# Kernel tuning notes

Measured on AMD Instinct MI355X. Metric: run time of the kernel, lower is better.

The kernel has to match this reference:

```python
import jax, jax.numpy as jnp
import numpy as np

B, T, I, H, O = 64, 1024, 256, 512, 128


def setup_inputs() -> dict:
    key = jax.random.key(0)
    ks = jax.random.split(key, 12)
    s = 1.0 / np.sqrt(H)  # PyTorch LSTM init: U(-1/sqrt(H), 1/sqrt(H))
    u = lambda k, shape: jax.random.uniform(k, shape, jnp.float32, -s, s)
    return {
        "inputs": jax.random.normal(ks[0], (B, T, I), jnp.float32),
        "W_ih_f": u(ks[1], (4 * H, I)),
        "W_hh_f": u(ks[2], (4 * H, H)),
        "b_ih_f": u(ks[3], (4 * H,)),
        "b_hh_f": u(ks[4], (4 * H,)),
        "W_ih_b": u(ks[5], (4 * H, I)),
        "W_hh_b": u(ks[6], (4 * H, H)),
        "b_ih_b": u(ks[7], (4 * H,)),
        "b_hh_b": u(ks[8], (4 * H,)),
        "W_out": u(ks[9], (O, 2 * H)),
        "b_out": u(ks[10], (O,)),
    }


def _lstm_dir(inputs, W_ih, W_hh, b_ih, b_hh, reverse):
    # Precompute input contribution for all timesteps: [B,T,4H] -> [T,B,4H]
    xg = jnp.einsum("bti,gi->btg", inputs, W_ih) + b_ih + b_hh
    xg = jnp.swapaxes(xg, 0, 1)
    b = inputs.shape[0]
    h0 = jnp.zeros((b, H), inputs.dtype)
    c0 = jnp.zeros((b, H), inputs.dtype)

    def step(carry, x_t):
        h, c = carry
        gates = x_t + h @ W_hh.T  # [B,4H], PyTorch gate order i,f,g,o
        i, f, g, o = jnp.split(gates, 4, axis=-1)
        i = jax.nn.sigmoid(i)
        f = jax.nn.sigmoid(f)
        g = jnp.tanh(g)
        o = jax.nn.sigmoid(o)
        c = f * c + i * g
        h = o * jnp.tanh(c)
        return (h, c), h

    (hT, cT), hs = jax.lax.scan(step, (h0, c0), xg, reverse=reverse)
    return jnp.swapaxes(hs, 0, 1), hT, cT  # hs: [B,T,H]


def reference(inputs, W_ih_f, W_hh_f, b_ih_f, b_hh_f,
              W_ih_b, W_hh_b, b_ih_b, b_hh_b, W_out, b_out):
    y_f, h_f, c_f = _lstm_dir(inputs, W_ih_f, W_hh_f, b_ih_f, b_hh_f, False)
    y_b, h_b, c_b = _lstm_dir(inputs, W_ih_b, W_hh_b, b_ih_b, b_hh_b, True)
    y = jnp.concatenate([y_f, y_b], axis=-1)            # [B,T,2H]
    out = jnp.einsum("bth,oh->bto", y, W_out) + b_out    # [B,T,O]
    h_n = jnp.stack([h_f, h_b])                          # [2,B,H]
    c_n = jnp.stack([c_f, c_b])                          # [2,B,H]
    return out, h_n, c_n
```

## Files before the change

### kernel.cpp

```cpp
#include <hip/hip_runtime.h>
#include <stdint.h>

#define T_LEN 1024
#define B_SZ  64
#define I_SZ  256
#define H_SZ  512
#define O_SZ  128

#define HB_OFF  0ull
#define Y_OFF   1048576ull
#define XBF_OFF 135266304ull
#define MEMSET_BYTES 1048576ull

typedef __attribute__((ext_vector_type(8))) short short8;
typedef __attribute__((ext_vector_type(4))) float f32x4;

__device__ __forceinline__ unsigned short f2bf(float f) {
  unsigned u = __float_as_uint(f);
  u += 0x7fffu + ((u >> 16) & 1u);
  return (unsigned short)(u >> 16);
}
__device__ __forceinline__ ushort4 cvt4(float4 v) {
  ushort4 p;
  p.x = f2bf(v.x); p.y = f2bf(v.y); p.z = f2bf(v.z); p.w = f2bf(v.w);
  return p;
}
__device__ __forceinline__ float sigm(float x) { return 1.0f / (1.0f + __expf(-x)); }
__device__ __forceinline__ float tanh_f(float x) { return 1.0f - 2.0f / (1.0f + __expf(2.0f * x)); }

__global__ void __launch_bounds__(256) cvt_x(const float* __restrict__ x,
                                             unsigned short* __restrict__ xb) {
  size_t i = ((size_t)blockIdx.x * 256 + threadIdx.x) * 8;
  float4 a = *(const float4*)(x + i);
  float4 b = *(const float4*)(x + i + 4);
  *(ushort4*)(xb + i)     = cvt4(a);
  *(ushort4*)(xb + i + 4) = cvt4(b);
}

__global__ void __launch_bounds__(512, 2)
lstm_scan(const unsigned short* __restrict__ xbf,
          const float* __restrict__ WihF, const float* __restrict__ WhhF,
          const float* __restrict__ bihF, const float* __restrict__ bhhF,
          const float* __restrict__ WihB, const float* __restrict__ WhhB,
          const float* __restrict__ bihB, const float* __restrict__ bhhB,
          unsigned char* __restrict__ ws, float* __restrict__ out)
{
  __shared__ unsigned short xs[2][16][264];
  __shared__ unsigned short hs[16][520];
  __shared__ float gbuf[4][16][36];
  __shared__ float cst[16][36];

  const int tid  = threadIdx.x;
  const int lane = tid & 63;
  const int wave = tid >> 6;
  const int nl   = lane & 15;
  const int q16  = lane >> 4;

  const int wg = blockIdx.x;
  const int d  = wg >> 6;
  const int b0 = ((wg >> 4) & 3) * 16;
  const int u0 = (wg & 15) * 32;

  const float* Wih = d ? WihB : WihF;
  const float* Whh = d ? WhhB : WhhF;
  const float* bih = d ? bihB : bihF;
  const float* bhh = d ? bhhB : bhhF;

  const int gate = wave >> 1;
  const int usub = (wave & 1) * 16;

  short8 wfrag[24];
  {
    const int row = gate * H_SZ + u0 + usub + nl;
    const float* wi = Wih + (size_t)row * I_SZ;
    const float* wh = Whh + (size_t)row * H_SZ;
#pragma unroll
    for (int kk = 0; kk < 24; ++kk) {
      const float* src = (kk < 8) ? (wi + kk * 32 + q16 * 8)
                                  : (wh + (kk - 8) * 32 + q16 * 8);
      float4 v0 = ((const float4*)src)[0];
      float4 v1 = ((const float4*)src)[1];
      short8 w;
      w[0] = (short)f2bf(v0.x); w[1] = (short)f2bf(v0.y);
      w[2] = (short)f2bf(v0.z); w[3] = (short)f2bf(v0.w);
      w[4] = (short)f2bf(v1.x); w[5] = (short)f2bf(v1.y);
      w[6] = (short)f2bf(v1.z); w[7] = (short)f2bf(v1.w);
      wfrag[kk] = w;
    }
  }
  const float bias = bih[gate * H_SZ + u0 + usub + nl] + bhh[gate * H_SZ + u0 + usub + nl];

  cst[tid >> 5][tid & 31] = 0.0f;

  unsigned* hbuf32 = (unsigned*)(ws + HB_OFF);
  unsigned* ybuf32 = (unsigned*)(ws + Y_OFF);
  unsigned* hs32   = (unsigned*)hs;

  const int sm = tid >> 5, sseg = tid & 31;

  {
    const int t0 = d ? (T_LEN - 1) : 0;
    uint4 a = *(const uint4*)(xbf + ((size_t)(b0 + sm) * T_LEN + t0) * I_SZ + sseg * 8);
    *(uint4*)(&xs[0][sm][sseg * 8]) = a;
  }
  __syncthreads();
  f32x4 xacc = {0.f, 0.f, 0.f, 0.f};
  {
    const unsigned short* xr = &xs[0][nl][q16 * 8];
#pragma unroll
    for (int kk = 0; kk < 8; ++kk) {
      short8 a = *(const short8*)(xr + kk * 32);
      xacc = __builtin_amdgcn_mfma_f32_16x16x32_bf16(a, wfrag[kk], xacc, 0, 0, 0);
    }
  }
  uint4 px;
  {
    const int t1 = d ? (T_LEN - 2) : 1;
    px = *(const uint4*)(xbf + ((size_t)(b0 + sm) * T_LEN + t1) * I_SZ + sseg * 8);
  }

  for (int s = 0; s < T_LEN; ++s) {
    const int t   = d ? (T_LEN - 1 - s) : s;
    const int cur = s & 1, nxt = cur ^ 1;
    const int rb  = cur ^ 1, wb = cur;

    unsigned wlo[8], whi[8];
    const unsigned* hb = hbuf32 + (size_t)((rb * 2 + d) * B_SZ + b0) * 512;
#pragma unroll
    for (int j = 0; j < 8; ++j) {
      int lin2 = j * 512 + tid;
      int m = lin2 >> 8, p = lin2 & 255;
      wlo[j] = __hip_atomic_load(hb + m * 512 + 2 * p,     __ATOMIC_RELAXED, __HIP_MEMORY_SCOPE_AGENT);
      whi[j] = __hip_atomic_load(hb + m * 512 + 2 * p + 1, __ATOMIC_RELAXED, __HIP_MEMORY_SCOPE_AGENT);
    }
    if (s < T_LEN - 1)
      *(uint4*)(&xs[nxt][sm][sseg * 8]) = px;
    {
      const unsigned tag = (unsigned)s;
      for (;;) {
        unsigned bad = 0;
#pragma unroll
        for (int j = 0; j < 8; ++j)
          bad |= (((wlo[j] ^ tag) | (whi[j] ^ tag)) & 0xffffu) ? (1u << j) : 0u;
        if (!bad) break;
#pragma unroll
        for (int j = 0; j < 8; ++j)
          if (bad & (1u << j)) {
            int lin2 = j * 512 + tid;
            int m = lin2 >> 8, p = lin2 & 255;
            wlo[j] = __hip_atomic_load(hb + m * 512 + 2 * p,     __ATOMIC_RELAXED, __HIP_MEMORY_SCOPE_AGENT);
            whi[j] = __hip_atomic_load(hb + m * 512 + 2 * p + 1, __ATOMIC_RELAXED, __HIP_MEMORY_SCOPE_AGENT);
          }
      }
    }
#pragma unroll
    for (int j = 0; j < 8; ++j) {
      int lin2 = j * 512 + tid;
      int m = lin2 >> 8, p = lin2 & 255;
      hs32[m * 260 + p] = (wlo[j] >> 16) | (whi[j] & 0xffff0000u);
    }
    __syncthreads();

    f32x4 acc0 = xacc, acc1 = {0.f, 0.f, 0.f, 0.f};
    {
      const unsigned short* ar = &hs[nl][q16 * 8];
#pragma unroll
      for (int kk = 0; kk < 16; kk += 2) {
        short8 a0 = *(const short8*)(ar + kk * 32);
        short8 a1 = *(const short8*)(ar + (kk + 1) * 32);
        acc0 = __builtin_amdgcn_mfma_f32_16x16x32_bf16(a0, wfrag[8 + kk], acc0, 0, 0, 0);
        acc1 = __builtin_amdgcn_mfma_f32_16x16x32_bf16(a1, wfrag[9 + kk], acc1, 0, 0, 0);
      }
      acc0 += acc1;
    }

#pragma unroll
    for (int r = 0; r < 4; ++r) {
      float v = acc0[r] + bias;
      v = (gate == 2) ? tanh_f(v) : sigm(v);
      gbuf[gate][q16 * 4 + r][usub + nl] = v;
    }
    __syncthreads();

    {
      int m = tid >> 5, n = tid & 31;
      float gi = gbuf[0][m][n], gf = gbuf[1][m][n];
      float gg = gbuf[2][m][n], go = gbuf[3][m][n];
      float c = gf * cst[m][n] + gi * gg;
      cst[m][n] = c;
      float h = go * tanh_f(c);
      unsigned hbits = f2bf(h);
      __hip_atomic_store(hbuf32 + (size_t)((wb * 2 + d) * B_SZ + b0 + m) * 512 + u0 + n,
                         (hbits << 16) | (unsigned)(s + 1),
                         __ATOMIC_RELAXED, __HIP_MEMORY_SCOPE_AGENT);
      unsigned other = __shfl_xor(hbits, 1);
      if ((tid & 1) == 0) {
        unsigned packed = hbits | (other << 16);
        size_t yi = ((size_t)(b0 + m) * T_LEN + t) * 512 + (d * H_SZ + u0 + n) / 2;
        ybuf32[yi] = packed;
      }
      if (s == T_LEN - 1) {
        size_t hi = (size_t)(d * B_SZ + b0 + m) * H_SZ + u0 + n;
        out[8388608ull + hi] = h;
        out[8388608ull + 65536ull + hi] = c;
      }
    }

    if (s < T_LEN - 1) {
      if (s + 2 < T_LEN) {
        const int t2 = d ? (T_LEN - 3 - s) : (s + 2);
        px = *(const uint4*)(xbf + ((size_t)(b0 + sm) * T_LEN + t2) * I_SZ + sseg * 8);
      }
      f32x4 xa = {0.f, 0.f, 0.f, 0.f};
      const unsigned short* xr = &xs[nxt][nl][q16 * 8];
#pragma unroll
      for (int kk = 0; kk < 8; ++kk) {
        short8 a = *(const short8*)(xr + kk * 32);
        xa = __builtin_amdgcn_mfma_f32_16x16x32_bf16(a, wfrag[kk], xa, 0, 0, 0);
      }
      xacc = xa;
    }
  }
}

__global__ void __launch_bounds__(256, 1)
proj(const unsigned short* __restrict__ y, const float* __restrict__ Wout,
     const float* __restrict__ bout, float* __restrict__ out)
{
  __shared__ unsigned short ys[128 * 264];
  __shared__ unsigned short wst[128 * 264];

  const int tid  = threadIdx.x;
  const int wave = tid >> 6;
  const int lane = tid & 63;
  const int nl   = lane & 15;
  const int q16  = lane >> 4;
  const int m0   = blockIdx.x * 128;

  f32x4 acc[2][8];
#pragma unroll
  for (int a = 0; a < 2; ++a)
#pragma unroll
    for (int b = 0; b < 8; ++b) acc[a][b] = (f32x4){0.f, 0.f, 0.f, 0.f};

  for (int k0 = 0; k0 < 1024; k0 += 256) {
    {
      int r = tid >> 1, half = tid & 1;
      const uint4* src = (const uint4*)(y + (size_t)(m0 + r) * 1024 + k0 + half * 128);
      uint4* dst = (uint4*)(ys + r * 264 + half * 128);
#pragma unroll
      for (int q = 0; q < 16; ++q) dst[q] = src[q];
    }
    {
      int r = tid >> 1, half = tid & 1;
      const float4* src = (const float4*)(Wout + (size_t)r * 1024 + k0 + half * 128);
      unsigned short* wd = wst + r * 264 + half * 128;
#pragma unroll
      for (int q = 0; q < 32; ++q) *(ushort4*)(wd + q * 4) = cvt4(src[q]);
    }
    __syncthreads();

#pragma unroll
    for (int kk = 0; kk < 8; ++kk) {
      const int ko = kk * 32 + q16 * 8;
      short8 bfr[8];
#pragma unroll
      for (int nt = 0; nt < 8; ++nt)
        bfr[nt] = *(const short8*)(wst + (nt * 16 + nl) * 264 + ko);
#pragma unroll
      for (int mtt = 0; mtt < 2; ++mtt) {
        short8 a = *(const short8*)(ys + ((wave * 2 + mtt) * 16 + nl) * 264 + ko);
#pragma unroll
        for (int nt = 0; nt < 8; ++nt)
          acc[mtt][nt] = __builtin_amdgcn_mfma_f32_16x16x32_bf16(a, bfr[nt], acc[mtt][nt], 0, 0, 0);
      }
    }
    __syncthreads();
  }

#pragma unroll
  for (int mtt = 0; mtt < 2; ++mtt) {
#pragma unroll
    for (int nt = 0; nt < 8; ++nt) {
      int col = nt * 16 + nl;
      float bo = bout[col];
      int rowb = m0 + (wave * 2 + mtt) * 16 + q16 * 4;
#pragma unroll
      for (int r = 0; r < 4; ++r)
        out[(size_t)(rowb + r) * O_SZ + col] = acc[mtt][nt][r] + bo;
    }
  }
}

extern "C" void kernel_launch(void* const* d_in, const int* in_sizes, int n_in,
                              void* d_out, int out_size, void* d_ws, size_t ws_size,
                              hipStream_t stream) {
  const float* x    = (const float*)d_in[0];
  const float* WihF = (const float*)d_in[1];
  const float* WhhF = (const float*)d_in[2];
  const float* bihF = (const float*)d_in[3];
  const float* bhhF = (const float*)d_in[4];
  const float* WihB = (const float*)d_in[5];
  const float* WhhB = (const float*)d_in[6];
  const float* bihB = (const float*)d_in[7];
  const float* bhhB = (const float*)d_in[8];
  const float* Wout = (const float*)d_in[9];
  const float* bout = (const float*)d_in[10];
  float* out = (float*)d_out;
  unsigned char* ws = (unsigned char*)d_ws;

  hipMemsetAsync(ws, 0, (size_t)MEMSET_BYTES, stream);
  cvt_x<<<8192, 256, 0, stream>>>(x, (unsigned short*)(ws + XBF_OFF));
  lstm_scan<<<128, 512, 0, stream>>>((const unsigned short*)(ws + XBF_OFF),
                                     WihF, WhhF, bihF, bhhF,
                                     WihB, WhhB, bihB, bhhB,
                                     ws, out);
  proj<<<512, 256, 0, stream>>>((const unsigned short*)(ws + Y_OFF), Wout, bout, out);
}
```

Baseline: 3.267 ms.

## Interleave two batch halves per workgroup and shuffle gates in registers

Each workgroup now handles two 16-row batch halves in alternation, and the grid shrinks from 128 to 64 blocks. While one half waits on the cross-block h flags, the other half's recurrent GEMM and pointwise math can run, hiding the inter-block sync latency. Weight rows are reordered so the four gates of a unit fall in adjacent lanes and are combined with xor shuffles. This removes the gbuf shared-memory round trip, one barrier per step, and the x staging in LDS. The cost is half as many CUs doing twice the serial work per step, and a polling loop that now includes s_sleep.

```diff
diff --git a/kernel.cpp b/kernel.cpp
--- a/kernel.cpp
+++ b/kernel.cpp
@@ -45,33 +45,31 @@
           const float* __restrict__ bihB, const float* __restrict__ bhhB,
           unsigned char* __restrict__ ws, float* __restrict__ out)
 {
-  __shared__ unsigned short xs[2][16][264];
-  __shared__ unsigned short hs[16][520];
-  __shared__ float gbuf[4][16][36];
-  __shared__ float cst[16][36];
+  __shared__ unsigned short hs[2][16][520];
 
   const int tid  = threadIdx.x;
   const int lane = tid & 63;
   const int wave = tid >> 6;
   const int nl   = lane & 15;
   const int q16  = lane >> 4;
-
-  const int wg = blockIdx.x;
-  const int d  = wg >> 6;
-  const int b0 = ((wg >> 4) & 3) * 16;
-  const int u0 = (wg & 15) * 32;
+  const int uu   = nl >> 2;
+  const int gt   = nl & 3;
+  const int mrow = q16 * 4 + gt;
+
+  const int wg   = blockIdx.x;
+  const int d    = wg >> 5;
+  const int pair = (wg >> 4) & 1;
+  const int u0   = (wg & 15) * 32;
+  const int u    = u0 + wave * 4 + uu;
+  const int row  = gt * H_SZ + u;
 
   const float* Wih = d ? WihB : WihF;
   const float* Whh = d ? WhhB : WhhF;
   const float* bih = d ? bihB : bihF;
   const float* bhh = d ? bhhB : bhhF;
 
-  const int gate = wave >> 1;
-  const int usub = (wave & 1) * 16;
-
   short8 wfrag[24];
   {
-    const int row = gate * H_SZ + u0 + usub + nl;
     const float* wi = Wih + (size_t)row * I_SZ;
     const float* wh = Whh + (size_t)row * H_SZ;
 #pragma unroll
@@ -88,137 +86,147 @@
       wfrag[kk] = w;
     }
   }
-  const float bias = bih[gate * H_SZ + u0 + usub + nl] + bhh[gate * H_SZ + u0 + usub + nl];
-
-  cst[tid >> 5][tid & 31] = 0.0f;
+  const float bias = bih[row] + bhh[row];
 
   unsigned* hbuf32 = (unsigned*)(ws + HB_OFF);
   unsigned* ybuf32 = (unsigned*)(ws + Y_OFF);
-  unsigned* hs32   = (unsigned*)hs;
-
-  const int sm = tid >> 5, sseg = tid & 31;
-
-  {
+
+  const int b0h2[2] = { pair * 32, pair * 32 + 16 };
+  float cstr[2] = {0.f, 0.f};
+  f32x4 xacc[2];
+
+#pragma unroll
+  for (int half = 0; half < 2; ++half) {
     const int t0 = d ? (T_LEN - 1) : 0;
-    uint4 a = *(const uint4*)(xbf + ((size_t)(b0 + sm) * T_LEN + t0) * I_SZ + sseg * 8);
-    *(uint4*)(&xs[0][sm][sseg * 8]) = a;
-  }
-  __syncthreads();
-  f32x4 xacc = {0.f, 0.f, 0.f, 0.f};
-  {
-    const unsigned short* xr = &xs[0][nl][q16 * 8];
+    const unsigned short* xr =
+        xbf + ((size_t)(b0h2[half] + nl) * T_LEN + t0) * I_SZ + q16 * 8;
+    f32x4 xa = {0.f, 0.f, 0.f, 0.f};
 #pragma unroll
     for (int kk = 0; kk < 8; ++kk) {
       short8 a = *(const short8*)(xr + kk * 32);
-      xacc = __builtin_amdgcn_mfma_f32_16x16x32_bf16(a, wfrag[kk], xacc, 0, 0, 0);
-    }
-  }
-  uint4 px;
-  {
-    const int t1 = d ? (T_LEN - 2) : 1;
-    px = *(const uint4*)(xbf + ((size_t)(b0 + sm) * T_LEN + t1) * I_SZ + sseg * 8);
+      xa = __builtin_amdgcn_mfma_f32_16x16x32_bf16(a, wfrag[kk], xa, 0, 0, 0);
+    }
+    xacc[half] = xa;
+  }
+
+  unsigned wlo[8], whi[8];
+  const unsigned* hb = hbuf32 + (size_t)((1 * 2 + d) * B_SZ + b0h2[0]) * 512;
+#pragma unroll
+  for (int j = 0; j < 8; ++j) {
+    int lin2 = j * 512 + tid, mm = lin2 >> 8, pp = lin2 & 255;
+    wlo[j] = __hip_atomic_load(hb + mm * 512 + 2 * pp,     __ATOMIC_RELAXED, __HIP_MEMORY_SCOPE_AGENT);
+    whi[j] = __hip_atomic_load(hb + mm * 512 + 2 * pp + 1, __ATOMIC_RELAXED, __HIP_MEMORY_SCOPE_AGENT);
   }
 
   for (int s = 0; s < T_LEN; ++s) {
-    const int t   = d ? (T_LEN - 1 - s) : s;
-    const int cur = s & 1, nxt = cur ^ 1;
-    const int rb  = cur ^ 1, wb = cur;
-
-    unsigned wlo[8], whi[8];
-    const unsigned* hb = hbuf32 + (size_t)((rb * 2 + d) * B_SZ + b0) * 512;
-#pragma unroll
-    for (int j = 0; j < 8; ++j) {
-      int lin2 = j * 512 + tid;
-      int m = lin2 >> 8, p = lin2 & 255;
-      wlo[j] = __hip_atomic_load(hb + m * 512 + 2 * p,     __ATOMIC_RELAXED, __HIP_MEMORY_SCOPE_AGENT);
-      whi[j] = __hip_atomic_load(hb + m * 512 + 2 * p + 1, __ATOMIC_RELAXED, __HIP_MEMORY_SCOPE_AGENT);
-    }
-    if (s < T_LEN - 1)
-      *(uint4*)(&xs[nxt][sm][sseg * 8]) = px;
-    {
-      const unsigned tag = (unsigned)s;
-      for (;;) {
-        unsigned bad = 0;
-#pragma unroll
-        for (int j = 0; j < 8; ++j)
-          bad |= (((wlo[j] ^ tag) | (whi[j] ^ tag)) & 0xffffu) ? (1u << j) : 0u;
-        if (!bad) break;
-#pragma unroll
-        for (int j = 0; j < 8; ++j)
-          if (bad & (1u << j)) {
-            int lin2 = j * 512 + tid;
-            int m = lin2 >> 8, p = lin2 & 255;
-            wlo[j] = __hip_atomic_load(hb + m * 512 + 2 * p,     __ATOMIC_RELAXED, __HIP_MEMORY_SCOPE_AGENT);
-            whi[j] = __hip_atomic_load(hb + m * 512 + 2 * p + 1, __ATOMIC_RELAXED, __HIP_MEMORY_SCOPE_AGENT);
-          }
-      }
-    }
-#pragma unroll
-    for (int j = 0; j < 8; ++j) {
-      int lin2 = j * 512 + tid;
-      int m = lin2 >> 8, p = lin2 & 255;
-      hs32[m * 260 + p] = (wlo[j] >> 16) | (whi[j] & 0xffff0000u);
-    }
-    __syncthreads();
-
-    f32x4 acc0 = xacc, acc1 = {0.f, 0.f, 0.f, 0.f};
-    {
-      const unsigned short* ar = &hs[nl][q16 * 8];
-#pragma unroll
-      for (int kk = 0; kk < 16; kk += 2) {
-        short8 a0 = *(const short8*)(ar + kk * 32);
-        short8 a1 = *(const short8*)(ar + (kk + 1) * 32);
-        acc0 = __builtin_amdgcn_mfma_f32_16x16x32_bf16(a0, wfrag[8 + kk], acc0, 0, 0, 0);
-        acc1 = __builtin_amdgcn_mfma_f32_16x16x32_bf16(a1, wfrag[9 + kk], acc1, 0, 0, 0);
-      }
-      acc0 += acc1;
-    }
-
-#pragma unroll
-    for (int r = 0; r < 4; ++r) {
-      float v = acc0[r] + bias;
-      v = (gate == 2) ? tanh_f(v) : sigm(v);
-      gbuf[gate][q16 * 4 + r][usub + nl] = v;
-    }
-    __syncthreads();
-
-    {
-      int m = tid >> 5, n = tid & 31;
-      float gi = gbuf[0][m][n], gf = gbuf[1][m][n];
-      float gg = gbuf[2][m][n], go = gbuf[3][m][n];
-      float c = gf * cst[m][n] + gi * gg;
-      cst[m][n] = c;
-      float h = go * tanh_f(c);
+    const int t  = d ? (T_LEN - 1 - s) : s;
+    const int wb = s & 1;
+#pragma unroll
+    for (int half = 0; half < 2; ++half) {
+      const int b0 = b0h2[half];
+
+      short8 px[8];
+      if (s + 1 < T_LEN) {
+        const int tn = d ? (T_LEN - 2 - s) : (s + 1);
+        const unsigned short* xr =
+            xbf + ((size_t)(b0 + nl) * T_LEN + tn) * I_SZ + q16 * 8;
+#pragma unroll
+        for (int kk = 0; kk < 8; ++kk) px[kk] = *(const short8*)(xr + kk * 32);
+      }
+
+      {
+        const unsigned tag = (unsigned)s;
+        for (;;) {
+          unsigned bad = 0;
+#pragma unroll
+          for (int j = 0; j < 8; ++j)
+            bad |= (((wlo[j] ^ tag) | (whi[j] ^ tag)) & 0xffffu) ? (1u << j) : 0u;
+          if (!bad) break;
+          __builtin_amdgcn_s_sleep(1);
+#pragma unroll
+          for (int j = 0; j < 8; ++j)
+            if (bad & (1u << j)) {
+              int lin2 = j * 512 + tid, mm = lin2 >> 8, pp = lin2 & 255;
+              wlo[j] = __hip_atomic_load(hb + mm * 512 + 2 * pp,     __ATOMIC_RELAXED, __HIP_MEMORY_SCOPE_AGENT);
+              whi[j] = __hip_atomic_load(hb + mm * 512 + 2 * pp + 1, __ATOMIC_RELAXED, __HIP_MEMORY_SCOPE_AGENT);
+            }
+        }
+      }
+
+      {
+        unsigned* h32 = (unsigned*)&hs[half][0][0];
+#pragma unroll
+        for (int j = 0; j < 8; ++j) {
+          int lin2 = j * 512 + tid, mm = lin2 >> 8, pp = lin2 & 255;
+          h32[mm * 260 + pp] = (wlo[j] >> 16) | (whi[j] & 0xffff0000u);
+        }
+      }
+      __syncthreads();
+
+      f32x4 acc0 = xacc[half], acc1 = {0.f, 0.f, 0.f, 0.f};
+      {
+        const unsigned short* ar = &hs[half][nl][q16 * 8];
+#pragma unroll
+        for (int kk = 0; kk < 16; kk += 2) {
+          short8 a0 = *(const short8*)(ar + kk * 32);
+          short8 a1 = *(const short8*)(ar + (kk + 1) * 32);
+          acc0 = __builtin_amdgcn_mfma_f32_16x16x32_bf16(a0, wfrag[8 + kk], acc0, 0, 0, 0);
+          acc1 = __builtin_amdgcn_mfma_f32_16x16x32_bf16(a1, wfrag[9 + kk], acc1, 0, 0, 0);
+        }
+        acc0 += acc1;
+      }
+
+      float a0 = acc0[0] + bias, a1v = acc0[1] + bias;
+      float a2 = acc0[2] + bias, a3v = acc0[3] + bias;
+      float sh0 = __shfl_xor(a0, 1),  sh1 = __shfl_xor(a1v, 1);
+      float sh2 = __shfl_xor(a2, 1),  sh3 = __shfl_xor(a3v, 1);
+      float b0v, b1v, b2v, b3v;
+      if (lane & 1) { b0v = sh1; b1v = a1v; b2v = sh3; b3v = a3v; }
+      else          { b0v = a0;  b1v = sh0; b2v = a2;  b3v = sh2; }
+      float uh0 = __shfl_xor(b0v, 2), uh1 = __shfl_xor(b1v, 2);
+      float uh2 = __shfl_xor(b2v, 2), uh3 = __shfl_xor(b3v, 2);
+      float g_i, g_f, g_g, g_o;
+      if (lane & 2) { g_i = uh2; g_f = uh3; g_g = b2v; g_o = b3v; }
+      else          { g_i = b0v; g_f = b1v; g_g = uh0; g_o = uh1; }
+      g_i = sigm(g_i); g_f = sigm(g_f); g_g = tanh_f(g_g); g_o = sigm(g_o);
+      float c = g_f * cstr[half] + g_i * g_g;
+      cstr[half] = c;
+      float h = g_o * tanh_f(c);
       unsigned hbits = f2bf(h);
-      __hip_atomic_store(hbuf32 + (size_t)((wb * 2 + d) * B_SZ + b0 + m) * 512 + u0 + n,
+
+      __hip_atomic_store(hbuf32 + (size_t)((wb * 2 + d) * B_SZ + b0 + mrow) * 512 + u,
                          (hbits << 16) | (unsigned)(s + 1),
                          __ATOMIC_RELAXED, __HIP_MEMORY_SCOPE_AGENT);
-      unsigned other = __shfl_xor(hbits, 1);
-      if ((tid & 1) == 0) {
-        unsigned packed = hbits | (other << 16);
-        size_t yi = ((size_t)(b0 + m) * T_LEN + t) * 512 + (d * H_SZ + u0 + n) / 2;
-        ybuf32[yi] = packed;
+      unsigned other = __shfl_xor(hbits, 4);
+      if (((lane >> 2) & 1) == 0) {
+        size_t yi = ((size_t)(b0 + mrow) * T_LEN + t) * 512 + ((d * H_SZ + u) >> 1);
+        ybuf32[yi] = hbits | (other << 16);
       }
       if (s == T_LEN - 1) {
-        size_t hi = (size_t)(d * B_SZ + b0 + m) * H_SZ + u0 + n;
+        size_t hi = (size_t)(d * B_SZ + b0 + mrow) * H_SZ + u;
         out[8388608ull + hi] = h;
         out[8388608ull + 65536ull + hi] = c;
       }
-    }
-
-    if (s < T_LEN - 1) {
-      if (s + 2 < T_LEN) {
-        const int t2 = d ? (T_LEN - 3 - s) : (s + 2);
-        px = *(const uint4*)(xbf + ((size_t)(b0 + sm) * T_LEN + t2) * I_SZ + sseg * 8);
-      }
-      f32x4 xa = {0.f, 0.f, 0.f, 0.f};
-      const unsigned short* xr = &xs[nxt][nl][q16 * 8];
-#pragma unroll
-      for (int kk = 0; kk < 8; ++kk) {
-        short8 a = *(const short8*)(xr + kk * 32);
-        xa = __builtin_amdgcn_mfma_f32_16x16x32_bf16(a, wfrag[kk], xa, 0, 0, 0);
-      }
-      xacc = xa;
+
+      if (!(s == T_LEN - 1 && half == 1)) {
+        const int sn  = half ? (s + 1) : s;
+        const int rbn = (sn & 1) ^ 1;
+        hb = hbuf32 + (size_t)((rbn * 2 + d) * B_SZ + b0h2[half ^ 1]) * 512;
+#pragma unroll
+        for (int j = 0; j < 8; ++j) {
+          int lin2 = j * 512 + tid, mm = lin2 >> 8, pp = lin2 & 255;
+          wlo[j] = __hip_atomic_load(hb + mm * 512 + 2 * pp,     __ATOMIC_RELAXED, __HIP_MEMORY_SCOPE_AGENT);
+          whi[j] = __hip_atomic_load(hb + mm * 512 + 2 * pp + 1, __ATOMIC_RELAXED, __HIP_MEMORY_SCOPE_AGENT);
+        }
+      }
+
+      if (s + 1 < T_LEN) {
+        f32x4 xa = {0.f, 0.f, 0.f, 0.f};
+#pragma unroll
+        for (int kk = 0; kk < 8; ++kk)
+          xa = __builtin_amdgcn_mfma_f32_16x16x32_bf16(px[kk], wfrag[kk], xa, 0, 0, 0);
+        xacc[half] = xa;
+      }
     }
   }
 }
@@ -311,9 +319,9 @@
 
   hipMemsetAsync(ws, 0, (size_t)MEMSET_BYTES, stream);
   cvt_x<<<8192, 256, 0, stream>>>(x, (unsigned short*)(ws + XBF_OFF));
-  lstm_scan<<<128, 512, 0, stream>>>((const unsigned short*)(ws + XBF_OFF),
-                                     WihF, WhhF, bihF, bhhF,
-                                     WihB, WhhB, bihB, bhhB,
-                                     ws, out);
+  lstm_scan<<<64, 512, 0, stream>>>((const unsigned short*)(ws + XBF_OFF),
+                                    WihF, WhhF, bihF, bhhF,
+                                    WihB, WhhB, bihB, bhhB,
+                                    ws, out);
   proj<<<512, 256, 0, stream>>>((const unsigned short*)(ws + Y_OFF), Wout, bout, out);
 }
```

After: 9.894 ms. +202.8%, slower.
